# Kernel optimization log

Hardware: AMD Instinct MI355X
Metric: run time of the kernel (lower is better)

The kernel has to match this reference:

```python
import jax, jax.numpy as jnp
import numpy as np
from jax import lax

# config
DIM = 512
D_INNER = 1024
D_STATE = 16
D_CONV = 4
DT_RANK = 32
N_LAYERS = 4
NUM_CLASSES = 10
SEQ = 28
BATCH = 512
EPS = 1e-6


def setup_inputs() -> dict:
    key = jax.random.key(0)
    ks = iter(jax.random.split(key, 32))
    nrm = lambda shape, s=0.02: jax.random.normal(next(ks), shape, jnp.float32) * s
    L = N_LAYERS
    inp = {
        "x": jax.random.normal(next(ks), (BATCH, 1, 28, 28), jnp.float32),
        "row_proj_w": nrm((DIM, 28)),
        "row_proj_b": jnp.zeros((DIM,), jnp.float32),
        "norm_w": jnp.ones((L, DIM), jnp.float32),
        "in_proj_w": nrm((L, 2 * D_INNER, DIM)),
        "in_proj_b": jnp.zeros((L, 2 * D_INNER), jnp.float32),
        "conv_w": nrm((L, D_INNER, 1, D_CONV), 0.1),
        "conv_b": jnp.zeros((L, D_INNER), jnp.float32),
        "x_proj_w": nrm((L, DT_RANK + 2 * D_STATE, D_INNER)),
        "dt_proj_w": jax.random.uniform(next(ks), (L, D_INNER, DT_RANK), jnp.float32, -DT_RANK ** -0.5, DT_RANK ** -0.5),
        "dt_proj_b": nrm((L, D_INNER), 0.5),  # stands in for inverse-softplus dt init
        "A_log": jnp.broadcast_to(jnp.log(jnp.arange(1, D_STATE + 1, dtype=jnp.float32)), (L, D_INNER, D_STATE)).copy(),
        "D": jnp.ones((L, D_INNER), jnp.float32),
        "out_proj_w": nrm((L, DIM, D_INNER)),
        "out_proj_b": jnp.zeros((L, DIM), jnp.float32),
        "final_norm_w": jnp.ones((DIM,), jnp.float32),
        "cls_w": nrm((NUM_CLASSES, DIM)),
        "cls_b": jnp.zeros((NUM_CLASSES,), jnp.float32),
    }
    return inp


def _rmsnorm(x, w):
    rms = jnp.sqrt(jnp.mean(x * x, axis=-1, keepdims=True) + EPS)
    return x / rms * w


def _mamba_layer(h, in_w, in_b, cw, cb, xp_w, dtp_w, dtp_b, A_log, Dp, out_w, out_b):
    bsz, seq, _ = h.shape
    xz = h @ in_w.T + in_b                      # (B,S,2*d_inner)
    xpart, z = jnp.split(xz, 2, axis=-1)
    # depthwise causal conv1d (left pad d_conv-1 == truncation to seq_len)
    xc = lax.conv_general_dilated(
        xpart.transpose(0, 2, 1), cw, (1,), [(D_CONV - 1, 0)],
        feature_group_count=D_INNER) + cb[None, :, None]
    xc = jax.nn.silu(xc).transpose(0, 2, 1)      # (B,S,d_inner)
    xdb = xc @ xp_w.T                            # (B,S,dt_rank+2*d_state)
    dt, Bm, Cm = jnp.split(xdb, [DT_RANK, DT_RANK + D_STATE], axis=-1)
    dt = jax.nn.softplus(dt @ dtp_w.T + dtp_b)   # (B,S,d_inner)
    A = -jnp.exp(A_log)                          # (d_inner,d_state)

    def step(state, inp):
        xt, dtt, Bt, Ct = inp                    # (B,d),(B,d),(B,s),(B,s)
        dA = jnp.exp(dtt[:, :, None] * A)        # (B,d,s)
        state = state * dA + (dtt * xt)[:, :, None] * Bt[:, None, :]
        yt = jnp.einsum('bds,bs->bd', state, Ct)
        return state, yt

    xs = (xc.transpose(1, 0, 2), dt.transpose(1, 0, 2),
          Bm.transpose(1, 0, 2), Cm.transpose(1, 0, 2))
    init = jnp.zeros((bsz, D_INNER, D_STATE), xc.dtype)
    _, ys = lax.scan(step, init, xs)
    y = ys.transpose(1, 0, 2)                    # (B,S,d_inner)
    y = (y + Dp * xc) * jax.nn.silu(z)
    return y @ out_w.T + out_b


def reference(x, row_proj_w, row_proj_b, norm_w, in_proj_w, in_proj_b, conv_w,
              conv_b, x_proj_w, dt_proj_w, dt_proj_b, A_log, D, out_proj_w,
              out_proj_b, final_norm_w, cls_w, cls_b):
    bsz = x.shape[0]
    rows = x.reshape(bsz * SEQ, 28).astype(jnp.float32)
    h = (rows @ row_proj_w.T + row_proj_b).reshape(bsz, SEQ, DIM)
    for i in range(N_LAYERS):
        nh = _rmsnorm(h, norm_w[i])
        h = h + _mamba_layer(nh, in_proj_w[i], in_proj_b[i], conv_w[i], conv_b[i],
                             x_proj_w[i], dt_proj_w[i], dt_proj_b[i], A_log[i],
                             D[i], out_proj_w[i], out_proj_b[i])
    h = _rmsnorm(h, final_norm_w)
    return h[:, -1] @ cls_w.T + cls_b
```

## Files before the change

kernel.cpp:

```cpp
#include <hip/hip_runtime.h>
#include <hip/hip_bf16.h>

#define BATCHN 512
#define SEQL 28
#define DIMM 512
#define DINNER 1024
#define DSTATE 16
#define DTRANK 32
#define XDBW 64
#define EPSV 1e-6f
#define LDK 40
#define LOG2E 1.442695041f
#define LN2F 0.6931471806f

typedef __hip_bfloat16 bf16;
using f32x4 = __attribute__((ext_vector_type(4))) float;
using bf16x8 = __attribute__((ext_vector_type(8))) short;

typedef __attribute__((address_space(1))) const void* gas1_t;
typedef __attribute__((address_space(3))) void* las3_t;

__device__ __forceinline__ float lo16(unsigned u) {
    unsigned short h = (unsigned short)u; bf16 v = *(bf16*)&h; return __bfloat162float(v);
}
__device__ __forceinline__ float hi16(unsigned u) {
    unsigned short h = (unsigned short)(u >> 16); bf16 v = *(bf16*)&h; return __bfloat162float(v);
}
__device__ __forceinline__ float softplus_fast(float v) {
    return (v > 20.f) ? v : LN2F * __log2f(1.f + exp2f(v * LOG2E));
}

__global__ __launch_bounds__(256) void wcvt_kernel(const float* __restrict__ s,
                                                   bf16* __restrict__ d, int n) {
    int i = (blockIdx.x * 256 + threadIdx.x) * 8;
    if (i < n) {
        float4 a = *(const float4*)(s + i), b = *(const float4*)(s + i + 4);
        bf16 t[8];
        t[0] = __float2bfloat16(a.x); t[1] = __float2bfloat16(a.y);
        t[2] = __float2bfloat16(a.z); t[3] = __float2bfloat16(a.w);
        t[4] = __float2bfloat16(b.x); t[5] = __float2bfloat16(b.y);
        t[6] = __float2bfloat16(b.z); t[7] = __float2bfloat16(b.w);
        *(uint4*)(d + i) = *(uint4*)t;
    }
}

__global__ __launch_bounds__(256) void rp_kernel(const float* __restrict__ x,
                                                 const float* __restrict__ w,
                                                 const float* __restrict__ b,
                                                 float* __restrict__ h) {
    int row = blockIdx.x;
    int d = blockIdx.y * blockDim.x + threadIdx.x;
    __shared__ float xin[28];
    if (threadIdx.x < 28) xin[threadIdx.x] = x[row * 28 + threadIdx.x];
    __syncthreads();
    float acc = b[d];
#pragma unroll
    for (int k = 0; k < 28; ++k) acc = fmaf(w[d * 28 + k], xin[k], acc);
    h[(size_t)row * DIMM + d] = acc;
}

__global__ __launch_bounds__(256) void rmsn_kernel(const float* __restrict__ h,
                                                   const float* __restrict__ nw,
                                                   bf16* __restrict__ nh) {
    int row = blockIdx.x * blockDim.y + threadIdx.y;
    int lane = threadIdx.x;
    const float4* p = (const float4*)(h + (size_t)row * DIMM);
    float4 v0 = p[lane * 2], v1 = p[lane * 2 + 1];
    float ss = v0.x * v0.x + v0.y * v0.y + v0.z * v0.z + v0.w * v0.w +
               v1.x * v1.x + v1.y * v1.y + v1.z * v1.z + v1.w * v1.w;
#pragma unroll
    for (int off = 32; off > 0; off >>= 1) ss += __shfl_down(ss, off);
    ss = __shfl(ss, 0);
    float inv = rsqrtf(ss * (1.f / DIMM) + EPSV);
    const float4* wp = (const float4*)nw;
    float4 w0 = wp[lane * 2], w1 = wp[lane * 2 + 1];
    bf16 tmp[8];
    tmp[0] = __float2bfloat16(v0.x * inv * w0.x);
    tmp[1] = __float2bfloat16(v0.y * inv * w0.y);
    tmp[2] = __float2bfloat16(v0.z * inv * w0.z);
    tmp[3] = __float2bfloat16(v0.w * inv * w0.w);
    tmp[4] = __float2bfloat16(v1.x * inv * w1.x);
    tmp[5] = __float2bfloat16(v1.y * inv * w1.y);
    tmp[6] = __float2bfloat16(v1.z * inv * w1.z);
    tmp[7] = __float2bfloat16(v1.w * inv * w1.w);
    *(uint4*)(nh + (size_t)row * DIMM + lane * 8) = *(uint4*)tmp;
}

template <typename TC, int BM, int BN, bool ADDC, bool HASBIAS, int SPLITK, bool COAL>
__device__ __forceinline__ void gemm_core(char* smem,
                                          const bf16* __restrict__ A, int lda,
                                          const bf16* __restrict__ W,
                                          const float* __restrict__ bias,
                                          TC* __restrict__ C, int ldc,
                                          int Kfull, size_t c_split, int bz) {
    constexpr int BK = 32;
    constexpr int MI = (BN == 128) ? 4 : 1;
    constexpr int NI = 4;
    bf16* As = (bf16*)smem;
    bf16* Bs = As + BM * BK;
    const int t = threadIdx.x;
    const int w = t >> 6, l = t & 63;
    const int bm = blockIdx.x * BM;
    const int bn = blockIdx.y * BN;
    const int wm = (BN == 128) ? (w >> 1) * 64 : w * 16;
    const int wn = (BN == 128) ? (w & 1) * 64 : 0;
    const int Kloop = Kfull / SPLITK;
    const int kb = (SPLITK > 1) ? bz * Kloop : 0;
    if (SPLITK > 1) C += (size_t)bz * c_split;

    f32x4 acc[MI][NI] = {};
    constexpr int CHA = BM / 64;
    constexpr int CHB = BN / 64;
    const int lrow = l >> 2;
    const int lcol = (l & 3) * 8;

    for (int k0 = 0; k0 < Kloop; k0 += BK) {
        const int kcur = kb + k0;
        __syncthreads();
#pragma unroll
        for (int i = 0; i < CHA; ++i) {
            int chunk = w * CHA + i;
            int row = chunk * 16 + lrow;
            __builtin_amdgcn_global_load_lds(
                (gas1_t)(const void*)(A + (size_t)(bm + row) * lda + kcur + lcol),
                (las3_t)(void*)(As + chunk * 512), 16, 0, 0);
        }
#pragma unroll
        for (int i = 0; i < CHB; ++i) {
            int chunk = w * CHB + i;
            int row = chunk * 16 + lrow;
            __builtin_amdgcn_global_load_lds(
                (gas1_t)(const void*)(W + (size_t)(bn + row) * Kfull + kcur + lcol),
                (las3_t)(void*)(Bs + chunk * 512), 16, 0, 0);
        }
        __syncthreads();
        bf16x8 af[MI], bfr[NI];
#pragma unroll
        for (int mi = 0; mi < MI; ++mi)
            af[mi] = *(const bf16x8*)(&As[(wm + mi * 16 + (l & 15)) * BK + (l >> 4) * 8]);
#pragma unroll
        for (int ni = 0; ni < NI; ++ni)
            bfr[ni] = *(const bf16x8*)(&Bs[(wn + ni * 16 + (l & 15)) * BK + (l >> 4) * 8]);
#pragma unroll
        for (int mi = 0; mi < MI; ++mi)
#pragma unroll
            for (int ni = 0; ni < NI; ++ni)
                acc[mi][ni] = __builtin_amdgcn_mfma_f32_16x16x32_bf16(af[mi], bfr[ni], acc[mi][ni], 0, 0, 0);
    }

    if constexpr (COAL && sizeof(TC) == 2) {
        __syncthreads();
        bf16* my = (bf16*)smem + w * (16 * 72);
        float bv[NI];
#pragma unroll
        for (int ni = 0; ni < NI; ++ni)
            bv[ni] = HASBIAS ? bias[bn + wn + ni * 16 + (l & 15)] : 0.f;
#pragma unroll
        for (int mi = 0; mi < MI; ++mi) {
#pragma unroll
            for (int ni = 0; ni < NI; ++ni)
#pragma unroll
                for (int r = 0; r < 4; ++r)
                    my[(((l >> 4) << 2) + r) * 72 + ni * 16 + (l & 15)] =
                        __float2bfloat16(acc[mi][ni][r] + bv[ni]);
            __syncthreads();
#pragma unroll
            for (int p = 0; p < 2; ++p) {
                int idx = p * 64 + l;
                int rr = idx >> 3, c8 = (idx & 7) * 8;
                uint4 vv = *(const uint4*)(&my[rr * 72 + c8]);
                *(uint4*)((bf16*)C + (size_t)(bm + wm + mi * 16 + rr) * ldc + bn + wn + c8) = vv;
            }
            __syncthreads();
        }
    } else if constexpr (COAL && sizeof(TC) == 4) {
        __syncthreads();
        float* myf = (float*)smem + w * (16 * 72);
        float bv[NI];
#pragma unroll
        for (int ni = 0; ni < NI; ++ni)
            bv[ni] = HASBIAS ? bias[bn + wn + ni * 16 + (l & 15)] : 0.f;
#pragma unroll
        for (int mi = 0; mi < MI; ++mi) {
#pragma unroll
            for (int ni = 0; ni < NI; ++ni)
#pragma unroll
                for (int r = 0; r < 4; ++r)
                    myf[(((l >> 4) << 2) + r) * 72 + ni * 16 + (l & 15)] = acc[mi][ni][r] + bv[ni];
            __syncthreads();
            int rr = l >> 2, c0 = l & 3;
            float* crow = (float*)C + (size_t)(bm + wm + mi * 16 + rr) * ldc + bn + wn;
#pragma unroll
            for (int c = 0; c < 4; ++c) {
                int slot = c0 + 4 * c;
                float4 v = *(float4*)(&myf[rr * 72 + slot * 4]);
                if (ADDC) {
                    float4 cc = *(const float4*)(crow + slot * 4);
                    v.x += cc.x; v.y += cc.y; v.z += cc.z; v.w += cc.w;
                }
                *(float4*)(crow + slot * 4) = v;
            }
            __syncthreads();
        }
    } else {
#pragma unroll
        for (int mi = 0; mi < MI; ++mi)
#pragma unroll
            for (int ni = 0; ni < NI; ++ni) {
                int col = bn + wn + ni * 16 + (l & 15);
                int rowb = bm + wm + mi * 16 + ((l >> 4) << 2);
                float bv = HASBIAS ? bias[col] : 0.f;
#pragma unroll
                for (int r = 0; r < 4; ++r) {
                    float v = acc[mi][ni][r] + bv;
                    size_t off = (size_t)(rowb + r) * ldc + col;
                    if (ADDC) v += ((float*)C)[off];
                    ((float*)C)[off] = v;
                }
            }
    }
}

__global__ __launch_bounds__(256) void g_inproj(const bf16* A, const bf16* W, const float* bias,
                                                bf16* C) {
    __shared__ char smem[16384];
    gemm_core<bf16, 128, 128, false, true, 1, true>(smem, A, DIMM, W, bias, C, 2 * DINNER, DIMM, 0, 0);
}
__global__ __launch_bounds__(256) void g_xdbk(const bf16* A, const bf16* W, float* C, size_t c_split) {
    __shared__ char smem[8192];
    gemm_core<float, 64, 64, false, false, 2, false>(smem, A, 2 * DINNER, W, nullptr, C, XDBW, DINNER,
                                                     c_split, blockIdx.z);
}
__global__ __launch_bounds__(256) void g_outproj(const bf16* A, const bf16* W, const float* bias,
                                                 float* C) {
    __shared__ char smem[18432];
    gemm_core<float, 128, 128, true, true, 1, true>(smem, A, 2 * DINNER, W, bias, C, DIMM, DINNER, 0, 0);
}

__global__ __launch_bounds__(256) void conv_kernel(bf16* __restrict__ xz,
                                                   const float* __restrict__ cw,
                                                   const float* __restrict__ cb) {
    int gid = blockIdx.x * blockDim.x + threadIdx.x;
    int b = gid >> 9, dp = gid & 511;
    int d = dp * 2;
    float4 wA = *(const float4*)(cw + d * 4);
    float4 wB = *(const float4*)(cw + d * 4 + 4);
    float bA = cb[d], bB = cb[d + 1];
    bf16* col = xz + (size_t)b * SEQL * (2 * DINNER) + d;
    float a0 = 0.f, a1 = 0.f, a2 = 0.f, b0 = 0.f, b1 = 0.f, b2 = 0.f;
#pragma unroll
    for (int t = 0; t < SEQL; ++t) {
        unsigned u = *(const unsigned*)(col + (size_t)t * (2 * DINNER));
        float a3 = lo16(u), b3 = hi16(u);
        float va = fmaf(wA.x, a0, fmaf(wA.y, a1, fmaf(wA.z, a2, fmaf(wA.w, a3, bA))));
        float vb = fmaf(wB.x, b0, fmaf(wB.y, b1, fmaf(wB.z, b2, fmaf(wB.w, b3, bB))));
        float sa = va * __builtin_amdgcn_rcpf(1.f + exp2f(-va * LOG2E));
        float sb = vb * __builtin_amdgcn_rcpf(1.f + exp2f(-vb * LOG2E));
        bf16 ra = __float2bfloat16(sa), rb = __float2bfloat16(sb);
        unsigned ur = ((unsigned)*(unsigned short*)&rb << 16) | *(unsigned short*)&ra;
        *(unsigned*)(col + (size_t)t * (2 * DINNER)) = ur;
        a0 = a1; a1 = a2; a2 = a3;
        b0 = b1; b1 = b2; b2 = b3;
    }
}

__global__ __launch_bounds__(128, 2) void scan_kernel(bf16* __restrict__ xz,
                                                      const float* __restrict__ xdb0,
                                                      const float* __restrict__ xdb1,
                                                      const float* __restrict__ dtw,
                                                      const float* __restrict__ dtb,
                                                      const float* __restrict__ A_log,
                                                      const float* __restrict__ Dp) {
    const int b = blockIdx.x >> 2;
    const int d0 = (blockIdx.x & 3) << 8;
    const int tid = threadIdx.x;
    const int w = tid >> 6, l = tid & 63;

    __shared__ bf16 ldt[SEQL][264];
    __shared__ bf16 lA[32][LDK];
    __shared__ float lBC[SEQL][36];

    const float* xr0 = xdb0 + (size_t)b * SEQL * XDBW;
    const float* xr1 = xdb1 + (size_t)b * SEQL * XDBW;

#pragma unroll
    for (int k = 0; k < 8; ++k) {
        int flat = k * 128 + tid;
        int t = flat >> 5, j = flat & 31;
        float v = (t < SEQL) ? xr0[t * XDBW + j] + xr1[t * XDBW + j] : 0.f;
        lA[t][j] = __float2bfloat16(v);
    }
#pragma unroll
    for (int k = 0; k < 7; ++k) {
        int idx = k * 128 + tid;
        int t = idx >> 5, j = idx & 31;
        lBC[t][j] = xr0[t * XDBW + 32 + j] + xr1[t * XDBW + 32 + j];
    }
    __syncthreads();

    {
        const int col = l & 15;
        const int ksl = (l >> 4) * 8;
        bf16x8 a0 = *(const bf16x8*)(&lA[col][ksl]);
        bf16x8 a1 = *(const bf16x8*)(&lA[16 + col][ksl]);
#pragma unroll
        for (int ni = 0; ni < 8; ++ni) {
            int dl = w * 128 + ni * 16 + col;
            const float* br = dtw + (size_t)(d0 + dl) * DTRANK + ksl;
            bf16x8 bv;
#pragma unroll
            for (int j = 0; j < 8; ++j) {
                bf16 xq = __float2bfloat16(br[j]);
                bv[j] = *(short*)&xq;
            }
            f32x4 acc0 = {}, acc1 = {};
            acc0 = __builtin_amdgcn_mfma_f32_16x16x32_bf16(a0, bv, acc0, 0, 0, 0);
            acc1 = __builtin_amdgcn_mfma_f32_16x16x32_bf16(a1, bv, acc1, 0, 0, 0);
            float bias = dtb[d0 + dl];
#pragma unroll
            for (int r = 0; r < 4; ++r) {
                int t0 = ((l >> 4) << 2) + r;
                ldt[t0][dl] = __float2bfloat16(softplus_fast(acc0[r] + bias));
                int t1 = 16 + t0;
                if (t1 < SEQL)
                    ldt[t1][dl] = __float2bfloat16(softplus_fast(acc1[r] + bias));
            }
        }
    }
    __syncthreads();

    const int dc = d0 + 2 * tid;
    float DdA = Dp[dc], DdB = Dp[dc + 1];
    bool fast = true;
#pragma unroll
    for (int s = 0; s < DSTATE; ++s) {
        float aA = __expf(A_log[(size_t)dc * DSTATE + s]);
        float aB = __expf(A_log[(size_t)(dc + 1) * DSTATE + s]);
        fast = fast && (__builtin_fabsf(aA - (float)(s + 1)) < 2e-3f)
                    && (__builtin_fabsf(aB - (float)(s + 1)) < 2e-3f);
    }

    bf16* xg = xz + (size_t)b * SEQL * (2 * DINNER) + dc;

    if (fast) {
        f32x4 sA[4] = {}, sB[4] = {};
        for (int t = 0; t < SEQL; ++t) {
            unsigned xu = *(const unsigned*)(xg + (size_t)t * (2 * DINNER));
            unsigned zu = *(const unsigned*)(xg + (size_t)t * (2 * DINNER) + DINNER);
            unsigned du = *(const unsigned*)(&ldt[t][2 * tid]);
            float dtA = lo16(du), dtB = hi16(du);
            float xA = lo16(xu), xB = hi16(xu);
            float zA = lo16(zu), zB = hi16(zu);
            float dxA = dtA * xA, dxB = dtB * xB;
            float qA = exp2f(-dtA * LOG2E), qB = exp2f(-dtB * LOG2E);
            float qA2 = qA * qA, qA4 = qA2 * qA2;
            float qB2 = qB * qB, qB4 = qB2 * qB2;
            f32x4 PA0; PA0[0] = qA; PA0[1] = qA2; PA0[2] = qA2 * qA; PA0[3] = qA4;
            f32x4 PB0; PB0[0] = qB; PB0[1] = qB2; PB0[2] = qB2 * qB; PB0[3] = qB4;
            const f32x4* Bp = (const f32x4*)&lBC[t][0];
            const f32x4* Cp = (const f32x4*)&lBC[t][16];
            f32x4 dxA4; dxA4[0] = dxA; dxA4[1] = dxA; dxA4[2] = dxA; dxA4[3] = dxA;
            f32x4 dxB4; dxB4[0] = dxB; dxB4[1] = dxB; dxB4[2] = dxB; dxB4[3] = dxB;
            f32x4 accA = {}, accB = {};
            f32x4 PA = PA0, PB = PB0;
#pragma unroll
            for (int i = 0; i < 4; ++i) {
                f32x4 Bv = Bp[i], Cv = Cp[i];
                sA[i] = sA[i] * PA + Bv * dxA4; accA += sA[i] * Cv;
                sB[i] = sB[i] * PB + Bv * dxB4; accB += sB[i] * Cv;
                if (i < 3) { PA = PA * qA4; PB = PB * qB4; }
            }
            float yA = accA[0] + accA[1] + accA[2] + accA[3];
            float yB = accB[0] + accB[1] + accB[2] + accB[3];
            float gA = zA * __builtin_amdgcn_rcpf(1.f + exp2f(-zA * LOG2E));
            float gB = zB * __builtin_amdgcn_rcpf(1.f + exp2f(-zB * LOG2E));
            bf16 oA = __float2bfloat16((yA + DdA * xA) * gA);
            bf16 oB = __float2bfloat16((yB + DdB * xB) * gB);
            unsigned ou = ((unsigned)*(unsigned short*)&oB << 16) | *(unsigned short*)&oA;
            *(unsigned*)(xg + (size_t)t * (2 * DINNER)) = ou;
        }
    } else {
        float AA[DSTATE], AB[DSTATE];
#pragma unroll
        for (int s = 0; s < DSTATE; ++s) {
            AA[s] = -__expf(A_log[(size_t)dc * DSTATE + s]) * LOG2E;
            AB[s] = -__expf(A_log[(size_t)(dc + 1) * DSTATE + s]) * LOG2E;
        }
        float sA[DSTATE] = {}, sB[DSTATE] = {};
        for (int t = 0; t < SEQL; ++t) {
            unsigned xu = *(const unsigned*)(xg + (size_t)t * (2 * DINNER));
            unsigned zu = *(const unsigned*)(xg + (size_t)t * (2 * DINNER) + DINNER);
            unsigned du = *(const unsigned*)(&ldt[t][2 * tid]);
            float dtA = lo16(du), dtB = hi16(du);
            float xA = lo16(xu), xB = hi16(xu);
            float zA = lo16(zu), zB = hi16(zu);
            float dxA = dtA * xA, dxB = dtB * xB;
            float yA = 0.f, yB = 0.f;
#pragma unroll
            for (int s = 0; s < DSTATE; ++s) {
                float Bv = lBC[t][s], Cv = lBC[t][16 + s];
                sA[s] = fmaf(sA[s], exp2f(dtA * AA[s]), dxA * Bv);
                sB[s] = fmaf(sB[s], exp2f(dtB * AB[s]), dxB * Bv);
                yA = fmaf(sA[s], Cv, yA);
                yB = fmaf(sB[s], Cv, yB);
            }
            float gA = zA * __builtin_amdgcn_rcpf(1.f + exp2f(-zA * LOG2E));
            float gB = zB * __builtin_amdgcn_rcpf(1.f + exp2f(-zB * LOG2E));
            bf16 oA = __float2bfloat16((yA + DdA * xA) * gA);
            bf16 oB = __float2bfloat16((yB + DdB * xB) * gB);
            unsigned ou = ((unsigned)*(unsigned short*)&oB << 16) | *(unsigned short*)&oA;
            *(unsigned*)(xg + (size_t)t * (2 * DINNER)) = ou;
        }
    }
}

__global__ __launch_bounds__(64) void head_kernel(const float* __restrict__ h,
                                                  const float* __restrict__ fw,
                                                  const float* __restrict__ clsw,
                                                  const float* __restrict__ clsb,
                                                  float* __restrict__ out) {
    int b = blockIdx.x;
    int lane = threadIdx.x;
    const float* row = h + ((size_t)b * SEQL + (SEQL - 1)) * DIMM;
    const float4* p = (const float4*)row;
    float4 v0 = p[lane * 2], v1 = p[lane * 2 + 1];
    float ss = v0.x * v0.x + v0.y * v0.y + v0.z * v0.z + v0.w * v0.w +
               v1.x * v1.x + v1.y * v1.y + v1.z * v1.z + v1.w * v1.w;
#pragma unroll
    for (int off = 32; off > 0; off >>= 1) ss += __shfl_down(ss, off);
    ss = __shfl(ss, 0);
    float inv = rsqrtf(ss * (1.f / DIMM) + EPSV);
    const float4* wp = (const float4*)fw;
    float4 w0 = wp[lane * 2], w1 = wp[lane * 2 + 1];
    float nv[8];
    nv[0] = v0.x * inv * w0.x; nv[1] = v0.y * inv * w0.y;
    nv[2] = v0.z * inv * w0.z; nv[3] = v0.w * inv * w0.w;
    nv[4] = v1.x * inv * w1.x; nv[5] = v1.y * inv * w1.y;
    nv[6] = v1.z * inv * w1.z; nv[7] = v1.w * inv * w1.w;
    for (int c = 0; c < 10; ++c) {
        const float* cr = clsw + (size_t)c * DIMM + lane * 8;
        float pacc = 0.f;
#pragma unroll
        for (int j = 0; j < 8; ++j) pacc = fmaf(nv[j], cr[j], pacc);
#pragma unroll
        for (int off = 32; off > 0; off >>= 1) pacc += __shfl_down(pacc, off);
        if (lane == 0) out[b * 10 + c] = pacc + clsb[c];
    }
}

extern "C" void kernel_launch(void* const* d_in, const int* in_sizes, int n_in,
                              void* d_out, int out_size, void* d_ws, size_t ws_size,
                              hipStream_t stream) {
    const float* x     = (const float*)d_in[0];
    const float* rpw   = (const float*)d_in[1];
    const float* rpb   = (const float*)d_in[2];
    const float* normw = (const float*)d_in[3];
    const float* inpw  = (const float*)d_in[4];
    const float* inpb  = (const float*)d_in[5];
    const float* convw = (const float*)d_in[6];
    const float* convb = (const float*)d_in[7];
    const float* xpw   = (const float*)d_in[8];
    const float* dtpw  = (const float*)d_in[9];
    const float* dtpb  = (const float*)d_in[10];
    const float* alog  = (const float*)d_in[11];
    const float* Dp    = (const float*)d_in[12];
    const float* outpw = (const float*)d_in[13];
    const float* outpb = (const float*)d_in[14];
    const float* fnw   = (const float*)d_in[15];
    const float* clsw  = (const float*)d_in[16];
    const float* clsb  = (const float*)d_in[17];
    float* out = (float*)d_out;

    const int n_in_w  = 4 * 2 * DINNER * DIMM;
    const int n_out_w = 4 * DIMM * DINNER;
    const int n_xp_w  = 4 * XDBW * DINNER;
    char* base = (char*)d_ws;
    bf16* wbf_in  = (bf16*)base; base += (size_t)n_in_w * 2;
    bf16* wbf_out = (bf16*)base; base += (size_t)n_out_w * 2;
    bf16* wbf_xp  = (bf16*)base; base += (size_t)n_xp_w * 2;
    const size_t fixed = (size_t)(n_in_w + n_out_w + n_xp_w) * 2;

    const size_t per_row = 512 * 4 + 512 * 2 + 2048 * 2 + 2 * 64 * 4;
    const int cand[5] = {512, 256, 128, 64, 32};
    int Bc = 32;
    for (int i = 0; i < 5; ++i) {
        size_t R = (size_t)cand[i] * SEQL;
        if (fixed + R * per_row + 4096 <= ws_size) { Bc = cand[i]; break; }
    }
    const int chunks = BATCHN / Bc;
    const int R = Bc * SEQL;

    float* h   = (float*)base; base += (size_t)R * DIMM * 4;
    bf16* nh   = (bf16*)base;  base += (size_t)R * DIMM * 2;
    bf16* xz   = (bf16*)base;  base += (size_t)R * 2 * DINNER * 2;
    float* xdb = (float*)base; base += (size_t)R * XDBW * 4 * 2;

    wcvt_kernel<<<n_in_w / (256 * 8), 256, 0, stream>>>(inpw, wbf_in, n_in_w);
    wcvt_kernel<<<n_out_w / (256 * 8), 256, 0, stream>>>(outpw, wbf_out, n_out_w);
    wcvt_kernel<<<n_xp_w / (256 * 8), 256, 0, stream>>>(xpw, wbf_xp, n_xp_w);

    for (int c = 0; c < chunks; ++c) {
        const int b0 = c * Bc;
        rp_kernel<<<dim3(R, DIMM / 256), 256, 0, stream>>>(
            x + (size_t)b0 * 784, rpw, rpb, h);

        for (int l = 0; l < 4; ++l) {
            rmsn_kernel<<<R / 4, dim3(64, 4), 0, stream>>>(h, normw + (size_t)l * DIMM, nh);

            g_inproj<<<dim3(R / 128, (2 * DINNER) / 128), 256, 0, stream>>>(
                nh, wbf_in + (size_t)l * 2 * DINNER * DIMM, inpb + (size_t)l * 2 * DINNER, xz);

            conv_kernel<<<(Bc * DINNER / 2) / 256, 256, 0, stream>>>(
                xz, convw + (size_t)l * DINNER * 4, convb + (size_t)l * DINNER);

            g_xdbk<<<dim3(R / 64, 1, 2), 256, 0, stream>>>(
                xz, wbf_xp + (size_t)l * XDBW * DINNER, xdb, (size_t)R * XDBW);

            scan_kernel<<<Bc * 4, 128, 0, stream>>>(
                xz, xdb, xdb + (size_t)R * XDBW,
                dtpw + (size_t)l * DINNER * DTRANK, dtpb + (size_t)l * DINNER,
                alog + (size_t)l * DINNER * DSTATE, Dp + (size_t)l * DINNER);

            g_outproj<<<dim3(R / 128, DIMM / 128), 256, 0, stream>>>(
                xz, wbf_out + (size_t)l * DIMM * DINNER, outpb + (size_t)l * DIMM, h);
        }
        head_kernel<<<Bc, 64, 0, stream>>>(h, fnw, clsw, clsb, out + (size_t)b0 * 10);
    }
}
```

Measured before the change: 736.2 us.

## Fuse depthwise conv+SiLU into x_proj GEMM prologue and scan kernel

Removes the standalone conv kernel that rewrote the x half of xz in place. The x_proj GEMM now builds its A tile by loading four time-shifted rows, applying the causal depthwise conv and SiLU, and writing bf16 to shared memory. The scan kernel recomputes the conv from raw values with a sliding window. This saves a full read-modify-write pass over the activations and one launch, at the cost of redundant conv math and four times the A-tile global loads in the GEMM.

```diff
diff --git a/kernel.cpp b/kernel.cpp
--- a/kernel.cpp
+++ b/kernel.cpp
@@ -28,6 +28,9 @@
 }
 __device__ __forceinline__ float softplus_fast(float v) {
     return (v > 20.f) ? v : LN2F * __log2f(1.f + exp2f(v * LOG2E));
+}
+__device__ __forceinline__ float silu_fast(float v) {
+    return v * __builtin_amdgcn_rcpf(1.f + exp2f(-v * LOG2E));
 }
 
 __global__ __launch_bounds__(256) void wcvt_kernel(const float* __restrict__ s,
@@ -86,13 +89,13 @@
     *(uint4*)(nh + (size_t)row * DIMM + lane * 8) = *(uint4*)tmp;
 }
 
-template <typename TC, int BM, int BN, bool ADDC, bool HASBIAS, int SPLITK, bool COAL>
+template <typename TC, int BM, int BN, bool ADDC, bool HASBIAS, bool COAL>
 __device__ __forceinline__ void gemm_core(char* smem,
                                           const bf16* __restrict__ A, int lda,
                                           const bf16* __restrict__ W,
                                           const float* __restrict__ bias,
                                           TC* __restrict__ C, int ldc,
-                                          int Kfull, size_t c_split, int bz) {
+                                          int Kfull) {
     constexpr int BK = 32;
     constexpr int MI = (BN == 128) ? 4 : 1;
     constexpr int NI = 4;
@@ -104,9 +107,6 @@
     const int bn = blockIdx.y * BN;
     const int wm = (BN == 128) ? (w >> 1) * 64 : w * 16;
     const int wn = (BN == 128) ? (w & 1) * 64 : 0;
-    const int Kloop = Kfull / SPLITK;
-    const int kb = (SPLITK > 1) ? bz * Kloop : 0;
-    if (SPLITK > 1) C += (size_t)bz * c_split;
 
     f32x4 acc[MI][NI] = {};
     constexpr int CHA = BM / 64;
@@ -114,15 +114,14 @@
     const int lrow = l >> 2;
     const int lcol = (l & 3) * 8;
 
-    for (int k0 = 0; k0 < Kloop; k0 += BK) {
-        const int kcur = kb + k0;
+    for (int k0 = 0; k0 < Kfull; k0 += BK) {
         __syncthreads();
 #pragma unroll
         for (int i = 0; i < CHA; ++i) {
             int chunk = w * CHA + i;
             int row = chunk * 16 + lrow;
             __builtin_amdgcn_global_load_lds(
-                (gas1_t)(const void*)(A + (size_t)(bm + row) * lda + kcur + lcol),
+                (gas1_t)(const void*)(A + (size_t)(bm + row) * lda + k0 + lcol),
                 (las3_t)(void*)(As + chunk * 512), 16, 0, 0);
         }
 #pragma unroll
@@ -130,7 +129,7 @@
             int chunk = w * CHB + i;
             int row = chunk * 16 + lrow;
             __builtin_amdgcn_global_load_lds(
-                (gas1_t)(const void*)(W + (size_t)(bn + row) * Kfull + kcur + lcol),
+                (gas1_t)(const void*)(W + (size_t)(bn + row) * Kfull + k0 + lcol),
                 (las3_t)(void*)(Bs + chunk * 512), 16, 0, 0);
         }
         __syncthreads();
@@ -202,65 +201,96 @@
             }
             __syncthreads();
         }
-    } else {
-#pragma unroll
-        for (int mi = 0; mi < MI; ++mi)
-#pragma unroll
-            for (int ni = 0; ni < NI; ++ni) {
-                int col = bn + wn + ni * 16 + (l & 15);
-                int rowb = bm + wm + mi * 16 + ((l >> 4) << 2);
-                float bv = HASBIAS ? bias[col] : 0.f;
-#pragma unroll
-                for (int r = 0; r < 4; ++r) {
-                    float v = acc[mi][ni][r] + bv;
-                    size_t off = (size_t)(rowb + r) * ldc + col;
-                    if (ADDC) v += ((float*)C)[off];
-                    ((float*)C)[off] = v;
-                }
-            }
     }
 }
 
 __global__ __launch_bounds__(256) void g_inproj(const bf16* A, const bf16* W, const float* bias,
                                                 bf16* C) {
     __shared__ char smem[16384];
-    gemm_core<bf16, 128, 128, false, true, 1, true>(smem, A, DIMM, W, bias, C, 2 * DINNER, DIMM, 0, 0);
-}
-__global__ __launch_bounds__(256) void g_xdbk(const bf16* A, const bf16* W, float* C, size_t c_split) {
-    __shared__ char smem[8192];
-    gemm_core<float, 64, 64, false, false, 2, false>(smem, A, 2 * DINNER, W, nullptr, C, XDBW, DINNER,
-                                                     c_split, blockIdx.z);
+    gemm_core<bf16, 128, 128, false, true, true>(smem, A, DIMM, W, bias, C, 2 * DINNER, DIMM);
 }
 __global__ __launch_bounds__(256) void g_outproj(const bf16* A, const bf16* W, const float* bias,
                                                  float* C) {
     __shared__ char smem[18432];
-    gemm_core<float, 128, 128, true, true, 1, true>(smem, A, 2 * DINNER, W, bias, C, DIMM, DINNER, 0, 0);
-}
-
-__global__ __launch_bounds__(256) void conv_kernel(bf16* __restrict__ xz,
-                                                   const float* __restrict__ cw,
-                                                   const float* __restrict__ cb) {
-    int gid = blockIdx.x * blockDim.x + threadIdx.x;
-    int b = gid >> 9, dp = gid & 511;
-    int d = dp * 2;
-    float4 wA = *(const float4*)(cw + d * 4);
-    float4 wB = *(const float4*)(cw + d * 4 + 4);
-    float bA = cb[d], bB = cb[d + 1];
-    bf16* col = xz + (size_t)b * SEQL * (2 * DINNER) + d;
-    float a0 = 0.f, a1 = 0.f, a2 = 0.f, b0 = 0.f, b1 = 0.f, b2 = 0.f;
-#pragma unroll
-    for (int t = 0; t < SEQL; ++t) {
-        unsigned u = *(const unsigned*)(col + (size_t)t * (2 * DINNER));
-        float a3 = lo16(u), b3 = hi16(u);
-        float va = fmaf(wA.x, a0, fmaf(wA.y, a1, fmaf(wA.z, a2, fmaf(wA.w, a3, bA))));
-        float vb = fmaf(wB.x, b0, fmaf(wB.y, b1, fmaf(wB.z, b2, fmaf(wB.w, b3, bB))));
-        float sa = va * __builtin_amdgcn_rcpf(1.f + exp2f(-va * LOG2E));
-        float sb = vb * __builtin_amdgcn_rcpf(1.f + exp2f(-vb * LOG2E));
-        bf16 ra = __float2bfloat16(sa), rb = __float2bfloat16(sb);
-        unsigned ur = ((unsigned)*(unsigned short*)&rb << 16) | *(unsigned short*)&ra;
-        *(unsigned*)(col + (size_t)t * (2 * DINNER)) = ur;
-        a0 = a1; a1 = a2; a2 = a3;
-        b0 = b1; b1 = b2; b2 = b3;
+    gemm_core<float, 128, 128, true, true, true>(smem, A, 2 * DINNER, W, bias, C, DIMM, DINNER);
+}
+
+__global__ __launch_bounds__(256) void g_xdbk(const bf16* __restrict__ xz,
+                                              const bf16* __restrict__ W,
+                                              const float* __restrict__ cw,
+                                              const float* __restrict__ cb,
+                                              float* __restrict__ C, size_t c_split) {
+    __shared__ bf16 As[64 * 32];
+    __shared__ bf16 Bs[64 * 32];
+    const int t = threadIdx.x;
+    const int w = t >> 6, l = t & 63;
+    const int bm = blockIdx.x * 64;
+    const int kb = blockIdx.z * 512;
+    float* Cp = C + (size_t)blockIdx.z * c_split;
+
+    const int arow = t >> 2;
+    const int akk = (t & 3) * 8;
+    const int grow = bm + arow;
+    const int tt = grow % SEQL;
+    const bf16* xr = xz + (size_t)grow * (2 * DINNER);
+
+    const int lrow = l >> 2, lcol = (l & 3) * 8;
+
+    f32x4 acc[4] = {};
+    const int wm = w * 16;
+
+    for (int k0 = 0; k0 < 512; k0 += 32) {
+        const int kcur = kb + k0;
+        __syncthreads();
+        {
+            const int dbase = kcur + akk;
+            uint4 z4; z4.x = z4.y = z4.z = z4.w = 0;
+            uint4 u3 = *(const uint4*)(xr + dbase);
+            uint4 u2 = (tt >= 1) ? *(const uint4*)(xr - 1 * (2 * DINNER) + dbase) : z4;
+            uint4 u1 = (tt >= 2) ? *(const uint4*)(xr - 2 * (2 * DINNER) + dbase) : z4;
+            uint4 u0 = (tt >= 3) ? *(const uint4*)(xr - 3 * (2 * DINNER) + dbase) : z4;
+            float f0[8], f1[8], f2[8], f3[8];
+            unsigned* p0 = (unsigned*)&u0; unsigned* p1 = (unsigned*)&u1;
+            unsigned* p2 = (unsigned*)&u2; unsigned* p3 = (unsigned*)&u3;
+#pragma unroll
+            for (int j = 0; j < 4; ++j) {
+                f0[2 * j] = lo16(p0[j]); f0[2 * j + 1] = hi16(p0[j]);
+                f1[2 * j] = lo16(p1[j]); f1[2 * j + 1] = hi16(p1[j]);
+                f2[2 * j] = lo16(p2[j]); f2[2 * j + 1] = hi16(p2[j]);
+                f3[2 * j] = lo16(p3[j]); f3[2 * j + 1] = hi16(p3[j]);
+            }
+            bf16 outv[8];
+#pragma unroll
+            for (int j = 0; j < 8; ++j) {
+                float4 wj = *(const float4*)(cw + (size_t)(dbase + j) * 4);
+                float v = fmaf(wj.x, f0[j], fmaf(wj.y, f1[j],
+                          fmaf(wj.z, f2[j], fmaf(wj.w, f3[j], cb[dbase + j]))));
+                outv[j] = __float2bfloat16(silu_fast(v));
+            }
+            *(uint4*)(&As[arow * 32 + akk]) = *(uint4*)outv;
+        }
+        {
+            int row = w * 16 + lrow;
+            __builtin_amdgcn_global_load_lds(
+                (gas1_t)(const void*)(W + (size_t)row * DINNER + kcur + lcol),
+                (las3_t)(void*)(Bs + w * 512), 16, 0, 0);
+        }
+        __syncthreads();
+        bf16x8 af = *(const bf16x8*)(&As[(wm + (l & 15)) * 32 + (l >> 4) * 8]);
+#pragma unroll
+        for (int ni = 0; ni < 4; ++ni) {
+            bf16x8 bfr = *(const bf16x8*)(&Bs[(ni * 16 + (l & 15)) * 32 + (l >> 4) * 8]);
+            acc[ni] = __builtin_amdgcn_mfma_f32_16x16x32_bf16(af, bfr, acc[ni], 0, 0, 0);
+        }
+    }
+
+#pragma unroll
+    for (int ni = 0; ni < 4; ++ni) {
+        int col = ni * 16 + (l & 15);
+        int rowb = bm + wm + ((l >> 4) << 2);
+#pragma unroll
+        for (int r = 0; r < 4; ++r)
+            Cp[(size_t)(rowb + r) * XDBW + col] = acc[ni][r];
     }
 }
 
@@ -269,6 +299,8 @@
                                                       const float* __restrict__ xdb1,
                                                       const float* __restrict__ dtw,
                                                       const float* __restrict__ dtb,
+                                                      const float* __restrict__ cw,
+                                                      const float* __restrict__ cb,
                                                       const float* __restrict__ A_log,
                                                       const float* __restrict__ Dp) {
     const int b = blockIdx.x >> 2;
@@ -331,6 +363,9 @@
 
     const int dc = d0 + 2 * tid;
     float DdA = Dp[dc], DdB = Dp[dc + 1];
+    float4 cwA = *(const float4*)(cw + (size_t)dc * 4);
+    float4 cwB = *(const float4*)(cw + (size_t)(dc + 1) * 4);
+    float cbA = cb[dc], cbB = cb[dc + 1];
     bool fast = true;
 #pragma unroll
     for (int s = 0; s < DSTATE; ++s) {
@@ -344,25 +379,31 @@
 
     if (fast) {
         f32x4 sA[4] = {}, sB[4] = {};
+        float wa0 = 0.f, wa1 = 0.f, wa2 = 0.f;
+        float wb0 = 0.f, wb1 = 0.f, wb2 = 0.f;
         for (int t = 0; t < SEQL; ++t) {
             unsigned xu = *(const unsigned*)(xg + (size_t)t * (2 * DINNER));
             unsigned zu = *(const unsigned*)(xg + (size_t)t * (2 * DINNER) + DINNER);
             unsigned du = *(const unsigned*)(&ldt[t][2 * tid]);
             float dtA = lo16(du), dtB = hi16(du);
-            float xA = lo16(xu), xB = hi16(xu);
+            float rA = lo16(xu), rB = hi16(xu);
+            float vA = fmaf(cwA.x, wa0, fmaf(cwA.y, wa1, fmaf(cwA.z, wa2, fmaf(cwA.w, rA, cbA))));
+            float vB = fmaf(cwB.x, wb0, fmaf(cwB.y, wb1, fmaf(cwB.z, wb2, fmaf(cwB.w, rB, cbB))));
+            float xA = silu_fast(vA), xB = silu_fast(vB);
+            wa0 = wa1; wa1 = wa2; wa2 = rA;
+            wb0 = wb1; wb1 = wb2; wb2 = rB;
             float zA = lo16(zu), zB = hi16(zu);
             float dxA = dtA * xA, dxB = dtB * xB;
             float qA = exp2f(-dtA * LOG2E), qB = exp2f(-dtB * LOG2E);
             float qA2 = qA * qA, qA4 = qA2 * qA2;
             float qB2 = qB * qB, qB4 = qB2 * qB2;
-            f32x4 PA0; PA0[0] = qA; PA0[1] = qA2; PA0[2] = qA2 * qA; PA0[3] = qA4;
-            f32x4 PB0; PB0[0] = qB; PB0[1] = qB2; PB0[2] = qB2 * qB; PB0[3] = qB4;
+            f32x4 PA; PA[0] = qA; PA[1] = qA2; PA[2] = qA2 * qA; PA[3] = qA4;
+            f32x4 PB; PB[0] = qB; PB[1] = qB2; PB[2] = qB2 * qB; PB[3] = qB4;
             const f32x4* Bp = (const f32x4*)&lBC[t][0];
             const f32x4* Cp = (const f32x4*)&lBC[t][16];
             f32x4 dxA4; dxA4[0] = dxA; dxA4[1] = dxA; dxA4[2] = dxA; dxA4[3] = dxA;
             f32x4 dxB4; dxB4[0] = dxB; dxB4[1] = dxB; dxB4[2] = dxB; dxB4[3] = dxB;
             f32x4 accA = {}, accB = {};
-            f32x4 PA = PA0, PB = PB0;
 #pragma unroll
             for (int i = 0; i < 4; ++i) {
                 f32x4 Bv = Bp[i], Cv = Cp[i];
@@ -387,12 +428,19 @@
             AB[s] = -__expf(A_log[(size_t)(dc + 1) * DSTATE + s]) * LOG2E;
         }
         float sA[DSTATE] = {}, sB[DSTATE] = {};
+        float wa0 = 0.f, wa1 = 0.f, wa2 = 0.f;
+        float wb0 = 0.f, wb1 = 0.f, wb2 = 0.f;
         for (int t = 0; t < SEQL; ++t) {
             unsigned xu = *(const unsigned*)(xg + (size_t)t * (2 * DINNER));
             unsigned zu = *(const unsigned*)(xg + (size_t)t * (2 * DINNER) + DINNER);
             unsigned du = *(const unsigned*)(&ldt[t][2 * tid]);
             float dtA = lo16(du), dtB = hi16(du);
-            float xA = lo16(xu), xB = hi16(xu);
+            float rA = lo16(xu), rB = hi16(xu);
+            float vA = fmaf(cwA.x, wa0, fmaf(cwA.y, wa1, fmaf(cwA.z, wa2, fmaf(cwA.w, rA, cbA))));
+            float vB = fmaf(cwB.x, wb0, fmaf(cwB.y, wb1, fmaf(cwB.z, wb2, fmaf(cwB.w, rB, cbB))));
+            float xA = silu_fast(vA), xB = silu_fast(vB);
+            wa0 = wa1; wa1 = wa2; wa2 = rA;
+            wb0 = wb1; wb1 = wb2; wb2 = rB;
             float zA = lo16(zu), zB = hi16(zu);
             float dxA = dtA * xA, dxB = dtB * xB;
             float yA = 0.f, yB = 0.f;
@@ -510,15 +558,15 @@
             g_inproj<<<dim3(R / 128, (2 * DINNER) / 128), 256, 0, stream>>>(
                 nh, wbf_in + (size_t)l * 2 * DINNER * DIMM, inpb + (size_t)l * 2 * DINNER, xz);
 
-            conv_kernel<<<(Bc * DINNER / 2) / 256, 256, 0, stream>>>(
-                xz, convw + (size_t)l * DINNER * 4, convb + (size_t)l * DINNER);
-
             g_xdbk<<<dim3(R / 64, 1, 2), 256, 0, stream>>>(
-                xz, wbf_xp + (size_t)l * XDBW * DINNER, xdb, (size_t)R * XDBW);
+                xz, wbf_xp + (size_t)l * XDBW * DINNER,
+                convw + (size_t)l * DINNER * 4, convb + (size_t)l * DINNER,
+                xdb, (size_t)R * XDBW);
 
             scan_kernel<<<Bc * 4, 128, 0, stream>>>(
                 xz, xdb, xdb + (size_t)R * XDBW,
                 dtpw + (size_t)l * DINNER * DTRANK, dtpb + (size_t)l * DINNER,
+                convw + (size_t)l * DINNER * 4, convb + (size_t)l * DINNER,
                 alog + (size_t)l * DINNER * DSTATE, Dp + (size_t)l * DINNER);
 
             g_outproj<<<dim3(R / 128, DIMM / 128), 256, 0, stream>>>(
```

New measurement: 985.6 us. 33.9% more time.
